# Kernel tuning notes

Hardware: AMD Instinct MI355X
Metric: run time of the kernel (lower is better)

## Reference

```python
import jax, jax.numpy as jnp
import numpy as np

D_MODEL, D_HEAD, N_HEAD, PERIOD = 1024, 64, 16, 30
B, T1, T2 = 2, 2048, 2048


def setup_inputs() -> dict:
    key = jax.random.key(0)
    ks = jax.random.split(key, 7)
    s_in = 1.0 / np.sqrt(D_MODEL)
    s_out = 1.0 / np.sqrt(N_HEAD * D_HEAD)
    return {
        "x": jax.random.normal(ks[0], (B, T1, D_MODEL), dtype=jnp.float32),
        "context": jax.random.normal(ks[1], (B, T2, D_MODEL), dtype=jnp.float32),
        "Wq": jax.random.uniform(ks[2], (N_HEAD * D_HEAD, D_MODEL), jnp.float32, -s_in, s_in),
        "Wk": jax.random.uniform(ks[3], (N_HEAD * D_HEAD, D_MODEL), jnp.float32, -s_in, s_in),
        "Wv": jax.random.uniform(ks[4], (N_HEAD * D_HEAD, D_MODEL), jnp.float32, -s_in, s_in),
        "Wo": jax.random.uniform(ks[5], (D_MODEL, N_HEAD * D_HEAD), jnp.float32, -s_out, s_out),
        "bo": jax.random.uniform(ks[6], (D_MODEL,), jnp.float32, -s_out, s_out),
    }


def reference(x, context, Wq, Wk, Wv, Wo, bo):
    Bx, T1x, _ = x.shape
    T2x = context.shape[1]
    scale = 1.0 / np.sqrt(D_HEAD).astype(np.float32)
    # projections (torch Linear: y = x @ W^T)
    q = (x @ Wq.T).reshape(Bx, T1x, N_HEAD, D_HEAD)
    k = (context @ Wk.T).reshape(Bx, T2x, N_HEAD, D_HEAD)
    v = (context @ Wv.T).reshape(Bx, T2x, N_HEAD, D_HEAD)
    # attention scores [B, H, T1, T2]
    scores = jnp.einsum('bihd,bjhd->bhij', q, k) * scale
    # ALiBi-style periodic distance bias
    dist = jnp.abs(jnp.arange(T1x)[:, None] - jnp.arange(T2x)[None, :])  # [T1,T2]
    bias = -(dist // PERIOD).astype(jnp.float32)                          # [T1,T2]
    head_scale = jnp.power(2.0, -jnp.arange(1, N_HEAD + 1, dtype=jnp.float32))
    biased = scores + bias[None, None, :, :] * head_scale[None, :, None, None]
    attn = jax.nn.softmax(biased, axis=-1)
    out = jnp.einsum('bhij,bjhd->bihd', attn, v).reshape(Bx, T1x, N_HEAD * D_HEAD)
    # output projection; dropout is identity in eval mode
    return out @ Wo.T + bo
```

## Files before the change

kernel.cpp:

```cpp
#include <hip/hip_runtime.h>
#include <hip/hip_fp16.h>

typedef _Float16 f16;
typedef __attribute__((ext_vector_type(8))) _Float16 f16x8;
typedef __attribute__((ext_vector_type(4))) _Float16 f16x4;
typedef __attribute__((ext_vector_type(2))) __fp16 fp16x2;
typedef __attribute__((ext_vector_type(4))) float f32x4;
typedef __attribute__((ext_vector_type(16))) float f32x16;

#define DM 1024
#define NH 16
#define DH 64
#define TT 2048
#define LOG2E 1.4426950408889634f
#define QSCALE 0.18033688f

#define SB0 __builtin_amdgcn_sched_barrier(0)
#define LGKM0 asm volatile("s_waitcnt lgkmcnt(0)" ::: "memory")

__global__ __launch_bounds__(256) void cvt_all(const float* __restrict__ x, const float* __restrict__ cx,
                                               const float* __restrict__ wq, const float* __restrict__ wk,
                                               const float* __restrict__ wv, const float* __restrict__ wo,
                                               f16* __restrict__ xb, f16* __restrict__ cb,
                                               f16* __restrict__ wqb, f16* __restrict__ wkb,
                                               f16* __restrict__ wvb, f16* __restrict__ wob,
                                               f16* __restrict__ FBf) {
  int idx = blockIdx.x * 256 + threadIdx.x;
  int stride = gridDim.x * 256;
  for (int i = idx; i < 3670016; i += stride) {
    if (i >= 3145728) {
      int c = i - 3145728;
      int half = c & 1, lane = (c >> 1) & 63, kvt = (c >> 7) & 63, qt = c >> 13;
      int qi = qt * 32 + (lane & 31);
      int jb = kvt * 32 + 16 * half + 8 * (lane >> 5);
      f16x8 v;
#pragma unroll
      for (int e = 0; e < 8; e++) {
        int d = qi - (jb + e); d = (d < 0) ? -d : d;
        v[e] = (f16)(d / 30);
      }
      reinterpret_cast<f16x8*>(FBf)[c] = v;
      continue;
    }
    const float* src; f16* dst; int off; float s = 1.0f;
    if (i < 2097152) {
      if (i < 1048576) { src = x; dst = xb; off = i; }
      else { src = cx; dst = cb; off = i - 1048576; }
    } else {
      int j = i - 2097152;
      int wsel = j >> 18;
      off = j & 262143;
      if (wsel == 0) { src = wq; dst = wqb; s = QSCALE; }
      else if (wsel == 1) { src = wk; dst = wkb; }
      else if (wsel == 2) { src = wv; dst = wvb; }
      else { src = wo; dst = wob; }
    }
    float4 v = reinterpret_cast<const float4*>(src)[off];
    f16x4 o = { (f16)(v.x * s), (f16)(v.y * s), (f16)(v.z * s), (f16)(v.w * s) };
    reinterpret_cast<f16x4*>(dst)[off] = o;
  }
}

__device__ __forceinline__ void gemm_mainloop(const f16* __restrict__ A, const f16* __restrict__ W,
                                              int bm, int bn, f16 (*As)[4096], f16 (*Bs)[4096],
                                              f32x4 (&acc)[4][4]) {
  int t = threadIdx.x;
  int w = t >> 6;
  int lane = t & 63, lr = lane & 15, g = lane >> 4;
  int wr = w >> 1, wc = w & 1;
  int scol = ((t & 3) ^ ((t >> 3) & 3)) * 8;
  const f16* a0 = A + (size_t)(bm + (t >> 2)) * DM + scol;
  const f16* a1 = a0 + (size_t)64 * DM;
  const f16* b0 = W + (size_t)(bn + (t >> 2)) * DM + scol;
  const f16* b1 = b0 + (size_t)64 * DM;
  int szg = ((lr >> 1) & 3) << 4;

  f16x8 rA0, rA1, rB0, rB1;
  auto LOADR = [&](int kt) {
    rA0 = *reinterpret_cast<const f16x8*>(a0 + kt);
    rA1 = *reinterpret_cast<const f16x8*>(a1 + kt);
    rB0 = *reinterpret_cast<const f16x8*>(b0 + kt);
    rB1 = *reinterpret_cast<const f16x8*>(b1 + kt);
  };
  auto WRITE = [&](int bufi) {
    char* Ab = (char*)As[bufi];
    char* Bb = (char*)Bs[bufi];
    *reinterpret_cast<f16x8*>(Ab + t * 16) = rA0;
    *reinterpret_cast<f16x8*>(Ab + 4096 + t * 16) = rA1;
    *reinterpret_cast<f16x8*>(Bb + t * 16) = rB0;
    *reinterpret_cast<f16x8*>(Bb + 4096 + t * 16) = rB1;
  };
  auto CMPG = [&](int bufi) {
    const char* Ab = (const char*)As[bufi];
    const char* Bb = (const char*)Bs[bufi];
    f16x8 af[4], bf[4];
#pragma unroll
    for (int mi = 0; mi < 4; mi++) {
      int row = wr * 64 + mi * 16 + lr;
      af[mi] = *reinterpret_cast<const f16x8*>(Ab + row * 64 + ((g << 4) ^ szg));
    }
#pragma unroll
    for (int ni = 0; ni < 4; ni++) {
      int row = wc * 64 + ni * 16 + lr;
      bf[ni] = *reinterpret_cast<const f16x8*>(Bb + row * 64 + ((g << 4) ^ szg));
    }
    __builtin_amdgcn_s_setprio(1);
#pragma unroll
    for (int mi = 0; mi < 4; mi++)
#pragma unroll
      for (int ni = 0; ni < 4; ni++)
        acc[mi][ni] = __builtin_amdgcn_mfma_f32_16x16x32_f16(af[mi], bf[ni], acc[mi][ni], 0, 0, 0);
    __builtin_amdgcn_s_setprio(0);
  };

  LOADR(0);
  WRITE(0);
  LOADR(32);
  LGKM0;
  __builtin_amdgcn_s_barrier();
  SB0;

#pragma unroll 1
  for (int tp = 0; tp < 16; tp++) {
    int s0 = 2 * tp;
    CMPG(0);
    WRITE(1);
    if (s0 + 2 < 32) LOADR((s0 + 2) * 32);
    LGKM0;
    __builtin_amdgcn_s_barrier();
    SB0;
    CMPG(1);
    if (s0 + 2 < 32) {
      WRITE(0);
      if (s0 + 3 < 32) LOADR((s0 + 3) * 32);
      LGKM0;
      __builtin_amdgcn_s_barrier();
      SB0;
    }
  }
}

__global__ __launch_bounds__(256) void qkv_gemm(const f16* __restrict__ xb, const f16* __restrict__ cb,
                                                const f16* __restrict__ wq, const f16* __restrict__ wk,
                                                const f16* __restrict__ wv,
                                                f16* __restrict__ Qo, f16* __restrict__ Ko,
                                                f16* __restrict__ Vt) {
  __shared__ f16 As[2][4096];
  __shared__ f16 Bs[2][4096];
  int gid = blockIdx.x >> 8;
  int bid = blockIdx.x & 255;
  int bm = (bid >> 3) * 128, bn = (bid & 7) * 128;
  const f16* A = (gid == 0) ? xb : cb;
  const f16* W = (gid == 0) ? wq : ((gid == 1) ? wk : wv);
  f32x4 acc[4][4] = {};
  gemm_mainloop(A, W, bm, bn, As, Bs, acc);

  int t = threadIdx.x, w = t >> 6, lane = t & 63, lr = lane & 15, g = lane >> 4;
  int wr = w >> 1, wc = w & 1;
  if (gid < 2) {
    f16* out = (gid == 0) ? Qo : Ko;
#pragma unroll
    for (int mi = 0; mi < 4; mi++) {
      int m0 = bm + wr * 64 + mi * 16 + 4 * g;
      int b = m0 >> 11, i0 = m0 & 2047;
#pragma unroll
      for (int ni = 0; ni < 4; ni++) {
        int n = bn + wc * 64 + ni * 16 + lr;
        int h = n >> 6, d = n & 63;
        size_t base = (((size_t)(b * NH + h)) * TT + i0) * DH + d;
#pragma unroll
        for (int r = 0; r < 4; r++)
          out[base + (size_t)r * DH] = (f16)acc[mi][ni][r];
      }
    }
  } else {
#pragma unroll
    for (int mi = 0; mi < 4; mi++) {
      int m0 = bm + wr * 64 + mi * 16 + 4 * g;
      int b = m0 >> 11, j0 = m0 & 2047;
#pragma unroll
      for (int ni = 0; ni < 4; ni++) {
        int n = bn + wc * 64 + ni * 16 + lr;
        int h = n >> 6, d = n & 63;
        f16x4 pk = { (f16)acc[mi][ni][0], (f16)acc[mi][ni][1],
                     (f16)acc[mi][ni][2], (f16)acc[mi][ni][3] };
        *reinterpret_cast<f16x4*>(&Vt[(((size_t)(b * NH + h)) * DH + d) * TT + j0]) = pk;
      }
    }
  }
}

__global__ __launch_bounds__(256) void out_gemm(const f16* __restrict__ Ob, const f16* __restrict__ wo,
                                                const float* __restrict__ bo, float* __restrict__ Y) {
  __shared__ f16 As[2][4096];
  __shared__ f16 Bs[2][4096];
  int bid = blockIdx.x;
  int bm = (bid >> 3) * 128, bn = (bid & 7) * 128;
  f32x4 acc[4][4] = {};
  gemm_mainloop(Ob, wo, bm, bn, As, Bs, acc);
  int t = threadIdx.x, w = t >> 6, lane = t & 63, lr = lane & 15, g = lane >> 4;
  int wr = w >> 1, wc = w & 1;
#pragma unroll
  for (int mi = 0; mi < 4; mi++) {
    int m0 = bm + wr * 64 + mi * 16 + 4 * g;
#pragma unroll
    for (int ni = 0; ni < 4; ni++) {
      int n = bn + wc * 64 + ni * 16 + lr;
      float bias = bo[n];
#pragma unroll
      for (int r = 0; r < 4; r++)
        Y[(size_t)(m0 + r) * DM + n] = acc[mi][ni][r] + bias;
    }
  }
}

struct FB4 { f16x8 a, b, c, d; };

__global__ __launch_bounds__(256, 2) void attn_kernel(const f16* __restrict__ Q, const f16* __restrict__ K,
                                                      const f16* __restrict__ V, const f16* __restrict__ FBf,
                                                      f16* __restrict__ O) {
  __shared__ f16 KV[2][8192];
  int o = blockIdx.x;
  int xcd = o & 7, idx = o >> 3;
  int bh = 4 * xcd + (idx >> 4), qblk = idx & 15;
  int h = bh & 15, b = bh >> 4;
  int tt = threadIdx.x, w = tt >> 6, lane = tt & 63;
  int col = lane & 31, hi = lane >> 5;
  int qi = qblk * 128 + w * 32 + col;

  const f16* qp = Q + ((size_t)bh * TT + qi) * DH + hi * 8;
  f16x8 qf[4];
#pragma unroll
  for (int s = 0; s < 4; s++) qf[s] = *reinterpret_cast<const f16x8*>(qp + 16 * s);

  const float nc2 = -exp2f(-(float)(h + 1)) * LOG2E;
  int qtp = qblk * 4 + w;
  const f16x8* fbp = reinterpret_cast<const f16x8*>(FBf) + ((size_t)qtp << 13) + (lane << 1);

  f32x4 rsv = { 0.f, 0.f, 0.f, 0.f };
  f32x16 oacc0 = {}, oacc1 = {};

  int rho0 = tt >> 3, G = tt & 7;
  int f0 = (rho0 & 7) ^ (3 * ((rho0 >> 4) & 1));
  int J0 = (rho0 & 19) | ((rho0 & 4) << 1) | ((rho0 & 8) >> 1);
  const f16* kp0 = K + ((size_t)bh * TT + J0) * DH + (G ^ f0) * 8;
  const f16* kp1 = K + ((size_t)bh * TT + 32 + J0) * DH + (G ^ f0) * 8;
  const f16* vp0 = V + ((size_t)bh * DH + rho0) * TT + (G ^ f0) * 8;
  const f16* vp1 = V + ((size_t)bh * DH + 32 + rho0) * TT + (G ^ f0) * 8;

  f16x8 r0, r1, r2, r3;
  auto LOADR = [&](int kv0) {
    r0 = *reinterpret_cast<const f16x8*>(kp0 + (size_t)kv0 * DH);
    r1 = *reinterpret_cast<const f16x8*>(kp1 + (size_t)kv0 * DH);
    r2 = *reinterpret_cast<const f16x8*>(vp0 + kv0);
    r3 = *reinterpret_cast<const f16x8*>(vp1 + kv0);
  };
  auto WRITE = [&](int bufi) {
    char* base = (char*)KV[bufi];
    *reinterpret_cast<f16x8*>(base + tt * 16) = r0;
    *reinterpret_cast<f16x8*>(base + 4096 + tt * 16) = r1;
    *reinterpret_cast<f16x8*>(base + 8192 + tt * 16) = r2;
    *reinterpret_cast<f16x8*>(base + 12288 + tt * 16) = r3;
  };

  int fcol = (col & 7) ^ (3 * ((col >> 4) & 1));
  int kb0 = col * 128;
  int ksw[4];
#pragma unroll
  for (int s = 0; s < 4; s++) ksw[s] = ((2 * s + hi) ^ fcol) << 4;

  auto FBLOAD = [&](int t) {
    FB4 f;
    f.a = fbp[256 * t];
    f.b = fbp[256 * t + 1];
    f.c = fbp[256 * t + 128];
    f.d = fbp[256 * t + 129];
    return f;
  };

  auto CMP = [&](int bufi, const FB4& fb) {
    const char* Kb = (const char*)KV[bufi];
    f32x16 S0 = {}, S1 = {};
    __builtin_amdgcn_s_setprio(1);
#pragma unroll
    for (int s = 0; s < 4; s++) {
      f16x8 ka0 = *reinterpret_cast<const f16x8*>(Kb + kb0 + ksw[s]);
      f16x8 ka1 = *reinterpret_cast<const f16x8*>(Kb + 4096 + kb0 + ksw[s]);
      S0 = __builtin_amdgcn_mfma_f32_32x32x16_f16(ka0, qf[s], S0, 0, 0, 0);
      S1 = __builtin_amdgcn_mfma_f32_32x32x16_f16(ka1, qf[s], S1, 0, 0, 0);
    }
    __builtin_amdgcn_s_setprio(0);
    float p0[16], p1[16];
#pragma unroll
    for (int r = 0; r < 16; r++) {
      float fb0 = (float)((r < 8) ? fb.a[r] : fb.b[r - 8]);
      float fb1 = (float)((r < 8) ? fb.c[r] : fb.d[r - 8]);
      p0[r] = __builtin_amdgcn_exp2f(fmaf(fb0, nc2, S0[r]));
      p1[r] = __builtin_amdgcn_exp2f(fmaf(fb1, nc2, S1[r]));
    }
#pragma unroll
    for (int r = 0; r < 4; r++) {
      f32x4 pa = { p0[4 * r], p0[4 * r + 1], p0[4 * r + 2], p0[4 * r + 3] };
      f32x4 pc = { p1[4 * r], p1[4 * r + 1], p1[4 * r + 2], p1[4 * r + 3] };
      rsv += pa + pc;
    }
    f16x8 pb[4];
#pragma unroll
    for (int s2 = 0; s2 < 2; s2++) {
      union { f16x8 v; fp16x2 hh[4]; } u0, u1;
#pragma unroll
      for (int q2 = 0; q2 < 4; q2++) {
        u0.hh[q2] = __builtin_amdgcn_cvt_pkrtz(p0[8 * s2 + 2 * q2], p0[8 * s2 + 2 * q2 + 1]);
        u1.hh[q2] = __builtin_amdgcn_cvt_pkrtz(p1[8 * s2 + 2 * q2], p1[8 * s2 + 2 * q2 + 1]);
      }
      pb[s2] = u0.v; pb[2 + s2] = u1.v;
    }
    __builtin_amdgcn_s_setprio(1);
#pragma unroll
    for (int s2 = 0; s2 < 4; s2++) {
      f16x8 va0 = *reinterpret_cast<const f16x8*>(Kb + 8192 + kb0 + ksw[s2]);
      f16x8 va1 = *reinterpret_cast<const f16x8*>(Kb + 12288 + kb0 + ksw[s2]);
      oacc0 = __builtin_amdgcn_mfma_f32_32x32x16_f16(va0, pb[s2], oacc0, 0, 0, 0);
      oacc1 = __builtin_amdgcn_mfma_f32_32x32x16_f16(va1, pb[s2], oacc1, 0, 0, 0);
    }
    __builtin_amdgcn_s_setprio(0);
  };

  LOADR(0);
  WRITE(0);
  LOADR(64);
  FB4 fA = FBLOAD(0);
  FB4 fB = FBLOAD(1);
  LGKM0;
  __builtin_amdgcn_s_barrier();
  SB0;

#pragma unroll 1
  for (int tp = 0; tp < 16; tp++) {
    int t0 = 2 * tp;
    CMP(0, fA);
    WRITE(1);
    if (t0 + 2 < 32) { LOADR((t0 + 2) << 6); fA = FBLOAD(t0 + 2); }
    LGKM0;
    __builtin_amdgcn_s_barrier();
    SB0;
    CMP(1, fB);
    if (t0 + 2 < 32) {
      WRITE(0);
      if (t0 + 3 < 32) { LOADR((t0 + 3) << 6); fB = FBLOAD(t0 + 3); }
      LGKM0;
      __builtin_amdgcn_s_barrier();
      SB0;
    }
  }

  float lsum = (rsv[0] + rsv[1]) + (rsv[2] + rsv[3]);
  lsum += __shfl_xor(lsum, 32, 64);
  float inv = __builtin_amdgcn_rcpf(lsum);

  size_t ob = ((size_t)b * TT + qi) * DM + h * DH + 4 * hi;
  const f32x16* oa[2] = { &oacc0, &oacc1 };
#pragma unroll
  for (int db = 0; db < 2; db++)
#pragma unroll
    for (int a = 0; a < 4; a++) {
      f16x4 o4 = { (f16)((*oa[db])[4 * a] * inv),     (f16)((*oa[db])[4 * a + 1] * inv),
                   (f16)((*oa[db])[4 * a + 2] * inv), (f16)((*oa[db])[4 * a + 3] * inv) };
      *reinterpret_cast<f16x4*>(&O[ob + 32 * db + 8 * a]) = o4;
    }
}

extern "C" void kernel_launch(void* const* d_in, const int* in_sizes, int n_in,
                              void* d_out, int out_size, void* d_ws, size_t ws_size,
                              hipStream_t stream) {
  const float* x  = (const float*)d_in[0];
  const float* cx = (const float*)d_in[1];
  const float* Wq = (const float*)d_in[2];
  const float* Wk = (const float*)d_in[3];
  const float* Wv = (const float*)d_in[4];
  const float* Wo = (const float*)d_in[5];
  const float* bo = (const float*)d_in[6];
  float* Y = (float*)d_out;

  const size_t NTOK = (size_t)2 * TT;
  f16* p = (f16*)d_ws;
  f16* xb  = p; p += NTOK * DM;
  f16* cb  = p; p += NTOK * DM;
  f16* wqb = p; p += (size_t)DM * DM;
  f16* wkb = p; p += (size_t)DM * DM;
  f16* wvb = p; p += (size_t)DM * DM;
  f16* wob = p; p += (size_t)DM * DM;
  f16* Qb  = p; p += NTOK * DM;
  f16* Kb  = p; p += NTOK * DM;
  f16* Vtb = p; p += NTOK * DM;
  f16* Ob  = p; p += NTOK * DM;
  f16* FBt = p;

  cvt_all<<<2048, 256, 0, stream>>>(x, cx, Wq, Wk, Wv, Wo, xb, cb, wqb, wkb, wvb, wob, FBt);
  qkv_gemm<<<768, 256, 0, stream>>>(xb, cb, wqb, wkb, wvb, Qb, Kb, Vtb);
  attn_kernel<<<512, 256, 0, stream>>>(Qb, Kb, Vtb, FBt, Ob);
  out_gemm<<<256, 256, 0, stream>>>(Ob, wob, bo, Y);
}
```

Baseline: 127.4 us.

## Fuse fp32-to-fp16 conversion into GEMM loads and drop separate convert pass

The standalone conversion kernel that wrote fp16 copies of x, context and all weights is removed. The GEMM mainloop is templated to load fp32 directly, convert in registers (applying the Q scale on the weight side) and store fp16 into shared memory. A small kernel still generates the bias-distance table. This removes a full read/write pass over inputs and weights, but each GEMM tile now reads twice the bytes from global memory and needs more registers for fp32 staging, and the weights are re-read in fp32 by many tiles.

```diff
diff --git a/kernel.cpp b/kernel.cpp
--- a/kernel.cpp
+++ b/kernel.cpp
@@ -18,77 +18,78 @@
 #define SB0 __builtin_amdgcn_sched_barrier(0)
 #define LGKM0 asm volatile("s_waitcnt lgkmcnt(0)" ::: "memory")
 
-__global__ __launch_bounds__(256) void cvt_all(const float* __restrict__ x, const float* __restrict__ cx,
-                                               const float* __restrict__ wq, const float* __restrict__ wk,
-                                               const float* __restrict__ wv, const float* __restrict__ wo,
-                                               f16* __restrict__ xb, f16* __restrict__ cb,
-                                               f16* __restrict__ wqb, f16* __restrict__ wkb,
-                                               f16* __restrict__ wvb, f16* __restrict__ wob,
-                                               f16* __restrict__ FBf) {
-  int idx = blockIdx.x * 256 + threadIdx.x;
-  int stride = gridDim.x * 256;
-  for (int i = idx; i < 3670016; i += stride) {
-    if (i >= 3145728) {
-      int c = i - 3145728;
-      int half = c & 1, lane = (c >> 1) & 63, kvt = (c >> 7) & 63, qt = c >> 13;
-      int qi = qt * 32 + (lane & 31);
-      int jb = kvt * 32 + 16 * half + 8 * (lane >> 5);
-      f16x8 v;
-#pragma unroll
-      for (int e = 0; e < 8; e++) {
-        int d = qi - (jb + e); d = (d < 0) ? -d : d;
-        v[e] = (f16)(d / 30);
-      }
-      reinterpret_cast<f16x8*>(FBf)[c] = v;
-      continue;
-    }
-    const float* src; f16* dst; int off; float s = 1.0f;
-    if (i < 2097152) {
-      if (i < 1048576) { src = x; dst = xb; off = i; }
-      else { src = cx; dst = cb; off = i - 1048576; }
-    } else {
-      int j = i - 2097152;
-      int wsel = j >> 18;
-      off = j & 262143;
-      if (wsel == 0) { src = wq; dst = wqb; s = QSCALE; }
-      else if (wsel == 1) { src = wk; dst = wkb; }
-      else if (wsel == 2) { src = wv; dst = wvb; }
-      else { src = wo; dst = wob; }
-    }
-    float4 v = reinterpret_cast<const float4*>(src)[off];
-    f16x4 o = { (f16)(v.x * s), (f16)(v.y * s), (f16)(v.z * s), (f16)(v.w * s) };
-    reinterpret_cast<f16x4*>(dst)[off] = o;
-  }
-}
-
-__device__ __forceinline__ void gemm_mainloop(const f16* __restrict__ A, const f16* __restrict__ W,
-                                              int bm, int bn, f16 (*As)[4096], f16 (*Bs)[4096],
-                                              f32x4 (&acc)[4][4]) {
+__global__ __launch_bounds__(256) void fbgen(f16* __restrict__ FBf) {
+  int c = blockIdx.x * 256 + threadIdx.x;
+  int half = c & 1, lane = (c >> 1) & 63, kvt = (c >> 7) & 63, qt = c >> 13;
+  int qi = qt * 32 + (lane & 31);
+  int jb = kvt * 32 + 16 * half + 8 * (lane >> 5);
+  f16x8 v;
+#pragma unroll
+  for (int e = 0; e < 8; e++) {
+    int d = qi - (jb + e); d = (d < 0) ? -d : d;
+    v[e] = (f16)(d / 30);
+  }
+  reinterpret_cast<f16x8*>(FBf)[c] = v;
+}
+
+__device__ __forceinline__ f16x8 cvt8rne(float4 a, float4 b, float s) {
+  f16x8 v;
+  v[0] = (f16)(a.x * s); v[1] = (f16)(a.y * s); v[2] = (f16)(a.z * s); v[3] = (f16)(a.w * s);
+  v[4] = (f16)(b.x * s); v[5] = (f16)(b.y * s); v[6] = (f16)(b.z * s); v[7] = (f16)(b.w * s);
+  return v;
+}
+
+template<bool A32, bool B32>
+__device__ __forceinline__ void gemm_mainloop_t(const void* Ap, const void* Wp,
+                                                int bm, int bn, float bscale,
+                                                f16 (*As)[4096], f16 (*Bs)[4096],
+                                                f32x4 (&acc)[4][4]) {
   int t = threadIdx.x;
   int w = t >> 6;
   int lane = t & 63, lr = lane & 15, g = lane >> 4;
   int wr = w >> 1, wc = w & 1;
   int scol = ((t & 3) ^ ((t >> 3) & 3)) * 8;
-  const f16* a0 = A + (size_t)(bm + (t >> 2)) * DM + scol;
-  const f16* a1 = a0 + (size_t)64 * DM;
-  const f16* b0 = W + (size_t)(bn + (t >> 2)) * DM + scol;
-  const f16* b1 = b0 + (size_t)64 * DM;
   int szg = ((lr >> 1) & 3) << 4;
 
-  f16x8 rA0, rA1, rB0, rB1;
+  const float* a32 = (const float*)Ap + (size_t)(bm + (t >> 2)) * DM + scol;
+  const f16*   a16 = (const f16*)Ap + (size_t)(bm + (t >> 2)) * DM + scol;
+  const float* b32 = (const float*)Wp + (size_t)(bn + (t >> 2)) * DM + scol;
+  const f16*   b16 = (const f16*)Wp + (size_t)(bn + (t >> 2)) * DM + scol;
+
+  float4 rAf[4], rBf[4];
+  f16x8 rA[2], rB[2];
+
   auto LOADR = [&](int kt) {
-    rA0 = *reinterpret_cast<const f16x8*>(a0 + kt);
-    rA1 = *reinterpret_cast<const f16x8*>(a1 + kt);
-    rB0 = *reinterpret_cast<const f16x8*>(b0 + kt);
-    rB1 = *reinterpret_cast<const f16x8*>(b1 + kt);
+    if constexpr (A32) {
+      rAf[0] = *reinterpret_cast<const float4*>(a32 + kt);
+      rAf[1] = *reinterpret_cast<const float4*>(a32 + kt + 4);
+      rAf[2] = *reinterpret_cast<const float4*>(a32 + (size_t)64 * DM + kt);
+      rAf[3] = *reinterpret_cast<const float4*>(a32 + (size_t)64 * DM + kt + 4);
+    } else {
+      rA[0] = *reinterpret_cast<const f16x8*>(a16 + kt);
+      rA[1] = *reinterpret_cast<const f16x8*>(a16 + (size_t)64 * DM + kt);
+    }
+    if constexpr (B32) {
+      rBf[0] = *reinterpret_cast<const float4*>(b32 + kt);
+      rBf[1] = *reinterpret_cast<const float4*>(b32 + kt + 4);
+      rBf[2] = *reinterpret_cast<const float4*>(b32 + (size_t)64 * DM + kt);
+      rBf[3] = *reinterpret_cast<const float4*>(b32 + (size_t)64 * DM + kt + 4);
+    } else {
+      rB[0] = *reinterpret_cast<const f16x8*>(b16 + kt);
+      rB[1] = *reinterpret_cast<const f16x8*>(b16 + (size_t)64 * DM + kt);
+    }
   };
   auto WRITE = [&](int bufi) {
     char* Ab = (char*)As[bufi];
     char* Bb = (char*)Bs[bufi];
-    *reinterpret_cast<f16x8*>(Ab + t * 16) = rA0;
-    *reinterpret_cast<f16x8*>(Ab + 4096 + t * 16) = rA1;
-    *reinterpret_cast<f16x8*>(Bb + t * 16) = rB0;
-    *reinterpret_cast<f16x8*>(Bb + 4096 + t * 16) = rB1;
+    f16x8 uA0 = A32 ? cvt8rne(rAf[0], rAf[1], 1.0f) : rA[0];
+    f16x8 uA1 = A32 ? cvt8rne(rAf[2], rAf[3], 1.0f) : rA[1];
+    f16x8 uB0 = B32 ? cvt8rne(rBf[0], rBf[1], bscale) : rB[0];
+    f16x8 uB1 = B32 ? cvt8rne(rBf[2], rBf[3], bscale) : rB[1];
+    *reinterpret_cast<f16x8*>(Ab + t * 16) = uA0;
+    *reinterpret_cast<f16x8*>(Ab + 4096 + t * 16) = uA1;
+    *reinterpret_cast<f16x8*>(Bb + t * 16) = uB0;
+    *reinterpret_cast<f16x8*>(Bb + 4096 + t * 16) = uB1;
   };
   auto CMPG = [&](int bufi) {
     const char* Ab = (const char*)As[bufi];
@@ -140,9 +141,9 @@
   }
 }
 
-__global__ __launch_bounds__(256) void qkv_gemm(const f16* __restrict__ xb, const f16* __restrict__ cb,
-                                                const f16* __restrict__ wq, const f16* __restrict__ wk,
-                                                const f16* __restrict__ wv,
+__global__ __launch_bounds__(256) void qkv_gemm(const float* __restrict__ x, const float* __restrict__ cx,
+                                                const float* __restrict__ wq, const float* __restrict__ wk,
+                                                const float* __restrict__ wv,
                                                 f16* __restrict__ Qo, f16* __restrict__ Ko,
                                                 f16* __restrict__ Vt) {
   __shared__ f16 As[2][4096];
@@ -150,10 +151,11 @@
   int gid = blockIdx.x >> 8;
   int bid = blockIdx.x & 255;
   int bm = (bid >> 3) * 128, bn = (bid & 7) * 128;
-  const f16* A = (gid == 0) ? xb : cb;
-  const f16* W = (gid == 0) ? wq : ((gid == 1) ? wk : wv);
+  const float* A = (gid == 0) ? x : cx;
+  const float* W = (gid == 0) ? wq : ((gid == 1) ? wk : wv);
+  float bscale = (gid == 0) ? QSCALE : 1.0f;
   f32x4 acc[4][4] = {};
-  gemm_mainloop(A, W, bm, bn, As, Bs, acc);
+  gemm_mainloop_t<true, true>(A, W, bm, bn, bscale, As, Bs, acc);
 
   int t = threadIdx.x, w = t >> 6, lane = t & 63, lr = lane & 15, g = lane >> 4;
   int wr = w >> 1, wc = w & 1;
@@ -190,14 +192,14 @@
   }
 }
 
-__global__ __launch_bounds__(256) void out_gemm(const f16* __restrict__ Ob, const f16* __restrict__ wo,
+__global__ __launch_bounds__(256) void out_gemm(const f16* __restrict__ Ob, const float* __restrict__ wo,
                                                 const float* __restrict__ bo, float* __restrict__ Y) {
   __shared__ f16 As[2][4096];
   __shared__ f16 Bs[2][4096];
   int bid = blockIdx.x;
   int bm = (bid >> 3) * 128, bn = (bid & 7) * 128;
   f32x4 acc[4][4] = {};
-  gemm_mainloop(Ob, wo, bm, bn, As, Bs, acc);
+  gemm_mainloop_t<false, true>(Ob, wo, bm, bn, 1.0f, As, Bs, acc);
   int t = threadIdx.x, w = t >> 6, lane = t & 63, lr = lane & 15, g = lane >> 4;
   int wr = w >> 1, wc = w & 1;
 #pragma unroll
@@ -384,20 +386,14 @@
 
   const size_t NTOK = (size_t)2 * TT;
   f16* p = (f16*)d_ws;
-  f16* xb  = p; p += NTOK * DM;
-  f16* cb  = p; p += NTOK * DM;
-  f16* wqb = p; p += (size_t)DM * DM;
-  f16* wkb = p; p += (size_t)DM * DM;
-  f16* wvb = p; p += (size_t)DM * DM;
-  f16* wob = p; p += (size_t)DM * DM;
   f16* Qb  = p; p += NTOK * DM;
   f16* Kb  = p; p += NTOK * DM;
   f16* Vtb = p; p += NTOK * DM;
   f16* Ob  = p; p += NTOK * DM;
   f16* FBt = p;
 
-  cvt_all<<<2048, 256, 0, stream>>>(x, cx, Wq, Wk, Wv, Wo, xb, cb, wqb, wkb, wvb, wob, FBt);
-  qkv_gemm<<<768, 256, 0, stream>>>(xb, cb, wqb, wkb, wvb, Qb, Kb, Vtb);
+  fbgen<<<2048, 256, 0, stream>>>(FBt);
+  qkv_gemm<<<768, 256, 0, stream>>>(x, cx, Wq, Wk, Wv, Qb, Kb, Vtb);
   attn_kernel<<<512, 256, 0, stream>>>(Qb, Kb, Vtb, FBt, Ob);
-  out_gemm<<<256, 256, 0, stream>>>(Ob, wob, bo, Y);
-}
+  out_gemm<<<256, 256, 0, stream>>>(Ob, Wo, bo, Y);
+}
```

Result: slower. 163.8 us (+28.5%).
